# Kernel tuning notes

Hardware: AMD Instinct MI355X
Metric: run time of the kernel (lower is better)

## Reference

```python
import jax, jax.numpy as jnp
import numpy as np

N, M, B = 50000, 400000, 1000   # nodes, edges, graphs
F, E, G, P = 39, 11, 200, 128   # node feat, edge feat, graph feat, predictor dim
T = 2                            # readout timesteps


def _leaky(x):
    return jnp.where(x > 0, x, 0.01 * x)  # nn.LeakyReLU default slope


def _gru(x, h, wih, whh, bih, bhh):
    # torch.nn.GRUCell math; weights stored [in, 3H] so we use x @ W
    gx = x @ wih + bih
    gh = h @ whh + bhh
    xr, xz, xn = jnp.split(gx, 3, axis=-1)
    hr, hz, hn = jnp.split(gh, 3, axis=-1)
    r = jax.nn.sigmoid(xr + hr)
    z = jax.nn.sigmoid(xz + hz)
    n = jnp.tanh(xn + r * hn)
    return (1.0 - z) * n + z * h


def _seg_softmax(logits, seg, num):
    # softmax over entries sharing the same segment id (dgl edge_softmax / softmax_nodes)
    m = jax.ops.segment_max(logits, seg, num_segments=num)
    e = jnp.exp(logits - m[seg])
    s = jax.ops.segment_sum(e, seg, num_segments=num)
    return e / s[seg]


def setup_inputs() -> dict:
    key = jax.random.key(0)
    kit = iter(jax.random.split(key, 64))

    def rn(shape, scale=0.1):
        return jax.random.normal(next(kit), shape, dtype=jnp.float32) * scale

    inp = dict(
        node_feats=rn((N, F), 1.0),
        edge_feats=rn((M, E), 1.0),
        pn_w=rn((F, G)), pn_b=rn((G,)),
        pe1_w=rn((F + E, G)), pe1_b=rn((G,)),
        pe2_w=rn((2 * G, 1)), pe2_b=rn((1,)),
        et_w=rn((G, G)), et_b=rn((G,)),
        gru0_wih=rn((G, 3 * G)), gru0_whh=rn((G, 3 * G)),
        gru0_bih=rn((3 * G,)), gru0_bhh=rn((3 * G,)),
        lpe_w=rn((2 * G, 1)), lpe_b=rn((1,)),
        lpn_w=rn((G, G)), lpn_b=rn((G,)),
        gru1_wih=rn((G, 3 * G)), gru1_whh=rn((G, 3 * G)),
        gru1_bih=rn((3 * G,)), gru1_bhh=rn((3 * G,)),
        r_logit_w=rn((T, 2 * G, 1)), r_logit_b=rn((T, 1)),
        r_proj_w=rn((T, G, G)), r_proj_b=rn((T, G)),
        r_gru_wih=rn((T, G, 3 * G)), r_gru_whh=rn((T, G, 3 * G)),
        r_gru_bih=rn((T, 3 * G)), r_gru_bhh=rn((T, 3 * G)),
        t_w=rn((G, P)), t_b=rn((P,)),
        src=jax.random.randint(next(kit), (M,), 0, N, dtype=jnp.int32),
        dst=jax.random.randint(next(kit), (M,), 0, N, dtype=jnp.int32),
        graph_ids=(jnp.arange(N, dtype=jnp.int32) // (N // B)).astype(jnp.int32),
    )
    return inp


def reference(node_feats, edge_feats,
              pn_w, pn_b, pe1_w, pe1_b, pe2_w, pe2_b, et_w, et_b,
              gru0_wih, gru0_whh, gru0_bih, gru0_bhh,
              lpe_w, lpe_b, lpn_w, lpn_b,
              gru1_wih, gru1_whh, gru1_bih, gru1_bhh,
              r_logit_w, r_logit_b, r_proj_w, r_proj_b,
              r_gru_wih, r_gru_whh, r_gru_bih, r_gru_bhh,
              t_w, t_b, src, dst, graph_ids):
    n = node_feats.shape[0]
    # ---- GetContext (first AttentiveFPGNN layer) ----
    hv_new = _leaky(node_feats @ pn_w + pn_b)                                   # [N,G]
    he1 = _leaky(jnp.concatenate([node_feats[src], edge_feats], -1) @ pe1_w + pe1_b)  # [M,G]
    logits = _leaky(jnp.concatenate([hv_new[dst], he1], -1) @ pe2_w + pe2_b)    # [M,1]
    a = _seg_softmax(logits, dst, n)
    c = jax.ops.segment_sum(a * (he1 @ et_w + et_b), dst, num_segments=n)       # [N,G]
    h = jax.nn.relu(_gru(jax.nn.elu(c), hv_new, gru0_wih, gru0_whh, gru0_bih, gru0_bhh))
    # ---- GNNLayer (num_layers-1 = 1) ----
    logits = _leaky(jnp.concatenate([h[dst], h[src]], -1) @ lpe_w + lpe_b)      # [M,1]
    a = _seg_softmax(logits, dst, n)
    hv_proj = h @ lpn_w + lpn_b
    c = jax.ops.segment_sum(a * hv_proj[src], dst, num_segments=n)
    h = jax.nn.relu(_gru(jax.nn.elu(c), h, gru1_wih, gru1_whh, gru1_bih, gru1_bhh))
    # ---- AttentiveFPReadout ----
    g = jax.ops.segment_sum(h, graph_ids, num_segments=B)                        # [B,G]
    for t in range(T):
        z = _leaky(jnp.concatenate([jax.nn.relu(g)[graph_ids], h], -1) @ r_logit_w[t] + r_logit_b[t])
        a = _seg_softmax(z, graph_ids, B)                                        # [N,1]
        hv = h @ r_proj_w[t] + r_proj_b[t]
        g_repr = jax.ops.segment_sum(a * hv, graph_ids, num_segments=B)
        g = _gru(jax.nn.elu(g_repr), g, r_gru_wih[t], r_gru_whh[t], r_gru_bih[t], r_gru_bhh[t])
    # ---- final transform ----
    return g @ t_w + t_b                                                         # [B,P]
```

## Files before the change

### kernel.cpp

```cpp
#include <hip/hip_runtime.h>
#include <hip/hip_bf16.h>

#define NN 50000
#define MM 400000
#define BB 1000
#define FF 39
#define EE 11
#define GG 200
#define PP 128

typedef __attribute__((ext_vector_type(8))) short bf16x8;
typedef __attribute__((ext_vector_type(4))) float f32x4;
struct us4 { unsigned short x, y, z, w; };

__device__ __forceinline__ float bf2f(unsigned short u) {
  return __uint_as_float(((unsigned int)u) << 16);
}
__device__ __forceinline__ unsigned short f2bf(float x) {
  union { __hip_bfloat16 b; unsigned short u; } v;
  v.b = __float2bfloat16(x);
  return v.u;
}
__device__ __forceinline__ float leakyf(float x) { return x > 0.f ? x : 0.01f * x; }
__device__ __forceinline__ float eluf(float x)   { return x > 0.f ? x : (expf(x) - 1.f); }
__device__ __forceinline__ float sigmf(float x)  { return 1.f / (1.f + expf(-x)); }
__device__ __forceinline__ int sw(int row, int seg) {
  return row * 32 + ((seg ^ ((row >> 1) & 3)) << 3);
}
template <typename T> __device__ __forceinline__ float ldv(const T* p);
template <> __device__ __forceinline__ float ldv<float>(const float* p) { return *p; }
template <> __device__ __forceinline__ float ldv<unsigned short>(const unsigned short* p) { return bf2f(*p); }

template <typename T>
__device__ __forceinline__ void stage16(const T* ap, int kbase, int K, bool rowok, short* tmp) {
  if (rowok && kbase + 16 <= K) {
    if constexpr (sizeof(T) == 2) {
      *(bf16x8*)&tmp[0] = *(const bf16x8*)(ap);
      *(bf16x8*)&tmp[8] = *(const bf16x8*)(ap + 8);
    } else {
#pragma unroll
      for (int j = 0; j < 16; ++j) tmp[j] = (short)f2bf(ap[j]);
    }
  } else if (rowok) {
#pragma unroll
    for (int j = 0; j < 16; ++j) {
      if (kbase + j < K) {
        if constexpr (sizeof(T) == 2) tmp[j] = (short)ap[j];
        else tmp[j] = (short)f2bf(ap[j]);
      } else tmp[j] = 0;
    }
  } else {
#pragma unroll
    for (int j = 0; j < 16; ++j) tmp[j] = 0;
  }
}

__global__ __launch_bounds__(256) void detect_dtype(const unsigned int* __restrict__ w,
                                                    int* __restrict__ flag) {
  __shared__ int cnt[256];
  int c = 0;
  for (int i = threadIdx.x; i < 2048; i += 256) {
    unsigned int e = (w[i] >> 8) & 0x7F;
    c += (e >= 60 && e <= 64) ? 1 : 0;
  }
  cnt[threadIdx.x] = c;
  __syncthreads();
  for (int s = 128; s; s >>= 1) {
    if (threadIdx.x < s) cnt[threadIdx.x] += cnt[threadIdx.x + s];
    __syncthreads();
  }
  if (threadIdx.x == 0) *flag = (cnt[0] >= 1024) ? 1 : 0;
}

struct CvtJob { const void* s; float* d; int n; int pad; };
struct CvtJobs32 { CvtJob j[32]; };

__global__ __launch_bounds__(256) void cvt_any(CvtJobs32 jobs, const int* __restrict__ flag) {
  CvtJob job = jobs.j[blockIdx.y];
  int isbf = *flag;
  if (isbf) {
    const unsigned short* s = (const unsigned short*)job.s;
    for (int i = blockIdx.x * 256 + threadIdx.x; i < job.n; i += gridDim.x * 256)
      job.d[i] = bf2f(s[i]);
  } else {
    const float* s = (const float*)job.s;
    for (int i = blockIdx.x * 256 + threadIdx.x; i < job.n; i += gridDim.x * 256)
      job.d[i] = s[i];
  }
}

struct TJob { const float* s; unsigned short* d; int K; int N; };
struct TJobs12 { TJob j[12]; };

__global__ __launch_bounds__(256) void transpose_bf16(TJobs12 jobs) {
  TJob job = jobs.j[blockIdx.y];
  int total = job.K * job.N;
  for (int idx = blockIdx.x * 256 + threadIdx.x; idx < total; idx += gridDim.x * 256) {
    int n = idx / job.K, k = idx - n * job.K;
    job.d[idx] = f2bf(job.s[(size_t)k * job.N + n]);
  }
}

__global__ __launch_bounds__(256) void hist_kernel(const int* __restrict__ dst,
                                                   int* __restrict__ cnt, int M) {
  int e = blockIdx.x * 256 + threadIdx.x;
  if (e < M) atomicAdd(&cnt[dst[e]], 1);
}

#define SCHUNK 2048
__global__ __launch_bounds__(256) void scan1_kernel(const int* __restrict__ cnt,
                                                    int* __restrict__ incl,
                                                    int* __restrict__ bsum, int n) {
  __shared__ int lds[256];
  int b = blockIdx.x, tid = threadIdx.x;
  int base = b * SCHUNK + tid * 8;
  int v[8], s = 0;
#pragma unroll
  for (int j = 0; j < 8; ++j) { int i = base + j; v[j] = (i < n) ? cnt[i] : 0; s += v[j]; }
  lds[tid] = s;
  __syncthreads();
  for (int o = 1; o < 256; o <<= 1) {
    int t = (tid >= o) ? lds[tid - o] : 0;
    __syncthreads();
    lds[tid] += t;
    __syncthreads();
  }
  int run = lds[tid] - s;
#pragma unroll
  for (int j = 0; j < 8; ++j) {
    run += v[j];
    int i = base + j;
    if (i < n) incl[i] = run;
  }
  if (tid == 255) bsum[b] = lds[255];
}

__global__ void scan2_kernel(int* __restrict__ bsum, int nb) {
  if (threadIdx.x == 0 && blockIdx.x == 0) {
    int run = 0;
    for (int i = 0; i < nb; ++i) { int t = bsum[i]; bsum[i] = run; run += t; }
  }
}

__global__ __launch_bounds__(256) void scan3_kernel(const int* __restrict__ incl,
                                                    const int* __restrict__ cnt,
                                                    const int* __restrict__ bsum,
                                                    int* __restrict__ offA,
                                                    int* __restrict__ cur, int n) {
  int i = blockIdx.x * 256 + threadIdx.x;
  if (i >= n) return;
  int o = incl[i] - cnt[i] + bsum[i / SCHUNK];
  offA[i] = o;
  cur[i] = o;
}

__global__ __launch_bounds__(256) void fill_kernel(const int* __restrict__ dst,
                                                   int* __restrict__ cur,
                                                   int* __restrict__ elist, int M) {
  int e = blockIdx.x * 256 + threadIdx.x;
  if (e >= M) return;
  int pos = atomicAdd(&cur[dst[e]], 1);
  elist[pos] = e;
}

__global__ __launch_bounds__(64) void l1_agg(
    const float* __restrict__ Xe, const unsigned short* __restrict__ xa,
    const unsigned short* __restrict__ hvnew,
    const float* __restrict__ pe1w_e, const float* __restrict__ pe1b,
    const float* __restrict__ pe2w_n, const float* __restrict__ pe2w_e,
    const float* __restrict__ pe2b, const int* __restrict__ srcA,
    const int* __restrict__ offA, const int* __restrict__ cntA, const int* __restrict__ elist,
    unsigned short* __restrict__ S, float* __restrict__ ssumOut, int N)
{
  int v = blockIdx.x;
  int lane = threadIdx.x;
  if (v >= N) return;
  int begin = offA[v], cnt = cntA[v];
  bool act = lane < 50;
  int kb = act ? 4 * lane : 0;
  float b[4], p[4], pn[4];
  float pw[EE][4];
#pragma unroll
// ... 70 lines not shown
    float h2 = bf2f(g0.z) + b[2], h3 = bf2f(g0.w) + b[3];
#pragma unroll
    for (int jj = 0; jj < EE; ++jj) {
      float x = Xe[(size_t)e0 * EE + jj];
      h0 += x * pw[jj][0]; h1 += x * pw[jj][1];
      h2 += x * pw[jj][2]; h3 += x * pw[jj][3];
    }
    h0 = leakyf(h0); h1 = leakyf(h1); h2 = leakyf(h2); h3 = leakyf(h3);
    float bp = h0 * p[0] + h1 * p[1] + h2 * p[2] + h3 * p[3];
#pragma unroll
    for (int o = 32; o; o >>= 1) bp += __shfl_down(bp, o);
    float w = __expf(fminf(leakyf(alv + __shfl(bp, 0)), 60.f));
    ss += w;
    a0 += w * h0; a1 += w * h1; a2 += w * h2; a3 += w * h3;
  }
  float inv = (cnt > 0) ? 1.f / ss : 0.f;
  if (act) {
    us4 o4;
    o4.x = f2bf(a0 * inv); o4.y = f2bf(a1 * inv);
    o4.z = f2bf(a2 * inv); o4.w = f2bf(a3 * inv);
    *(us4*)(S + (size_t)v * GG + kb) = o4;
  }
  if (lane == 0) ssumOut[v] = (cnt > 0) ? ss : 0.f;
}

__global__ __launch_bounds__(64) void l2_agg(
    const unsigned short* __restrict__ hvp, const float* __restrict__ gd,
    const float* __restrict__ gs, const float* __restrict__ lpeb,
    const int* __restrict__ srcA,
    const int* __restrict__ offA, const int* __restrict__ cntA, const int* __restrict__ elist,
    unsigned short* __restrict__ S2, int N)
{
  int v = blockIdx.x;
  int lane = threadIdx.x;
  if (v >= N) return;
  int begin = offA[v], cnt = cntA[v];
  bool act = lane < 50;
  int kb = act ? 4 * lane : 0;
  float gdv = gd[v] + lpeb[0];
  float ss = 0.f;
  float a0 = 0.f, a1 = 0.f, a2 = 0.f, a3 = 0.f;
  int t = 0;
  for (; t + 4 <= cnt; t += 4) {
    int e[4], s[4];
#pragma unroll
    for (int u = 0; u < 4; ++u) {
      e[u] = __builtin_amdgcn_readfirstlane(elist[begin + t + u]);
      s[u] = __builtin_amdgcn_readfirstlane(srcA[e[u]]);
    }
    us4 g0 = *(const us4*)(hvp + (size_t)s[0] * GG + kb);
    us4 g1 = *(const us4*)(hvp + (size_t)s[1] * GG + kb);
    us4 g2 = *(const us4*)(hvp + (size_t)s[2] * GG + kb);
    us4 g3 = *(const us4*)(hvp + (size_t)s[3] * GG + kb);
    float w0 = __expf(fminf(leakyf(gdv + gs[s[0]]), 60.f));
    float w1 = __expf(fminf(leakyf(gdv + gs[s[1]]), 60.f));
    float w2 = __expf(fminf(leakyf(gdv + gs[s[2]]), 60.f));
    float w3 = __expf(fminf(leakyf(gdv + gs[s[3]]), 60.f));
    ss += w0 + w1 + w2 + w3;
    a0 += w0 * bf2f(g0.x) + w1 * bf2f(g1.x) + w2 * bf2f(g2.x) + w3 * bf2f(g3.x);
    a1 += w0 * bf2f(g0.y) + w1 * bf2f(g1.y) + w2 * bf2f(g2.y) + w3 * bf2f(g3.y);
    a2 += w0 * bf2f(g0.z) + w1 * bf2f(g1.z) + w2 * bf2f(g2.z) + w3 * bf2f(g3.z);
    a3 += w0 * bf2f(g0.w) + w1 * bf2f(g1.w) + w2 * bf2f(g2.w) + w3 * bf2f(g3.w);
  }
  for (; t < cnt; ++t) {
    int e = __builtin_amdgcn_readfirstlane(elist[begin + t]);
    int s = __builtin_amdgcn_readfirstlane(srcA[e]);
    us4 g = *(const us4*)(hvp + (size_t)s * GG + kb);
    float w = __expf(fminf(leakyf(gdv + gs[s]), 60.f));
    ss += w;
    a0 += w * bf2f(g.x); a1 += w * bf2f(g.y);
    a2 += w * bf2f(g.z); a3 += w * bf2f(g.w);
  }
  float inv = (cnt > 0) ? 1.f / ss : 0.f;
  if (act) {
    us4 o4;
    o4.x = f2bf((cnt > 0) ? eluf(a0 * inv) : 0.f);
    o4.y = f2bf((cnt > 0) ? eluf(a1 * inv) : 0.f);
    o4.z = f2bf((cnt > 0) ? eluf(a2 * inv) : 0.f);
    o4.w = f2bf((cnt > 0) ? eluf(a3 * inv) : 0.f);
    *(us4*)(S2 + (size_t)v * GG + kb) = o4;
  }
}

template <typename TA>
__global__ __launch_bounds__(256) void mfma_gemm(
    const TA* __restrict__ A, const unsigned short* __restrict__ Wt,
    const float* __restrict__ bias, const float* __restrict__ rowmask,
    unsigned short* __restrict__ Cb, int Mr, int Nc, int K, int act)
{
  __shared__ __attribute__((aligned(16))) short As[128 * 32];
  __shared__ __attribute__((aligned(16))) short Bs[64 * 32];
  int ncol = (Nc + 63) >> 6;
  int nrowt = (Mr + 127) >> 7;
  int per = 8 * ncol;
  int grp = blockIdx.x / per, rem = blockIdx.x % per;
  int rowt = grp * 8 + (rem & 7), colt = rem >> 3;
  if (rowt >= nrowt) return;
  int row0 = rowt * 128, col0 = colt * 64;
  int tid = threadIdx.x;
  int w = tid >> 6, lane = tid & 63, quad = lane >> 4, l15 = lane & 15;

  f32x4 zero4 = {0.f, 0.f, 0.f, 0.f};
  f32x4 acc[2][4];
#pragma unroll
  for (int r = 0; r < 2; ++r)
#pragma unroll
    for (int c = 0; c < 4; ++c) acc[r][c] = zero4;

  for (int k0 = 0; k0 < K; k0 += 32) {
    {
      int row = tid >> 1, half = tid & 1;
      int r = row0 + row;
      short tmp[16];
      stage16<TA>(A + (size_t)r * K + k0 + half * 16, k0 + half * 16, K, r < Mr, tmp);
      *(bf16x8*)&As[sw(row, 2 * half)]     = *(bf16x8*)&tmp[0];
      *(bf16x8*)&As[sw(row, 2 * half + 1)] = *(bf16x8*)&tmp[8];
    }
    {
      int col = tid & 63, seg = tid >> 6;
      int n = col0 + col, k = k0 + seg * 8;
      short t8[8];
      const unsigned short* wp = Wt + (size_t)n * K + k;
      if (n < Nc && k + 8 <= K) {
        *(bf16x8*)&t8[0] = *(const bf16x8*)wp;
      } else {
#pragma unroll
        for (int j = 0; j < 8; ++j)
          t8[j] = (n < Nc && k + j < K) ? (short)wp[j] : (short)0;
      }
      *(bf16x8*)&Bs[sw(col, seg)] = *(bf16x8*)&t8[0];
    }
    __syncthreads();
    bf16x8 a[2], b[4];
#pragma unroll
    for (int r = 0; r < 2; ++r)
      a[r] = *(const bf16x8*)&As[sw(w * 32 + r * 16 + l15, quad)];
#pragma unroll
    for (int c = 0; c < 4; ++c)
      b[c] = *(const bf16x8*)&Bs[sw(c * 16 + l15, quad)];
#pragma unroll
    for (int r = 0; r < 2; ++r)
#pragma unroll
      for (int c = 0; c < 4; ++c)
        acc[r][c] = __builtin_amdgcn_mfma_f32_16x16x32_bf16(a[r], b[c], acc[r][c], 0, 0, 0);
    __syncthreads();
  }
#pragma unroll
  for (int r = 0; r < 2; ++r) {
#pragma unroll
    for (int c = 0; c < 4; ++c) {
      int col = col0 + c * 16 + l15;
      if (col >= Nc) continue;
#pragma unroll
      for (int i = 0; i < 4; ++i) {
        int row = row0 + w * 32 + r * 16 + quad * 4 + i;
        if (row >= Mr) continue;
        bool valid = (rowmask == nullptr) || (rowmask[row] > 0.f);
        float v = valid ? (acc[r][c][i] + (bias ? bias[col] : 0.f)) : 0.f;
        if (act == 1) v = leakyf(v);
        else if (act == 2) v = eluf(v);
        Cb[(size_t)row * Nc + col] = f2bf(v);
      }
    }
  }
}

template <typename TI, typename TO>
__global__ __launch_bounds__(256) void mfma_gru(
    const TI* __restrict__ X, const TI* __restrict__ H,
    const unsigned short* __restrict__ WtIH, const unsigned short* __restrict__ WtHH,
    const float* __restrict__ bih, const float* __restrict__ bhh,
    TO* __restrict__ Out, int R, int relu_out)
{
  __shared__ __attribute__((aligned(16))) short Xs[128 * 32];
  __shared__ __attribute__((aligned(16))) short Hs[128 * 32];
  __shared__ __attribute__((aligned(16))) short Ws[192 * 32];
  int nrowt = (R + 127) >> 7;
  int grp = blockIdx.x / 56, rem = blockIdx.x % 56;
  int rowt = grp * 8 + (rem & 7), colt = rem >> 3;
  if (rowt >= nrowt) return;
  int row0 = rowt * 128, col0 = colt * 32;
  int tid = threadIdx.x;
  int w = tid >> 6, lane = tid & 63, quad = lane >> 4, l15 = lane & 15;

  f32x4 zero4 = {0.f, 0.f, 0.f, 0.f};
  f32x4 acc[6][2][2];
#pragma unroll
  for (int g = 0; g < 6; ++g)
#pragma unroll
    for (int r = 0; r < 2; ++r)
#pragma unroll
      for (int c = 0; c < 2; ++c) acc[g][r][c] = zero4;

  for (int k0 = 0; k0 < GG; k0 += 32) {
    {
      int row = tid >> 1, half = tid & 1;
      int r = row0 + row;
      short tx[16], th[16];
      stage16<TI>(X + (size_t)r * GG + k0 + half * 16, k0 + half * 16, GG, r < R, tx);
      stage16<TI>(H + (size_t)r * GG + k0 + half * 16, k0 + half * 16, GG, r < R, th);
      *(bf16x8*)&Xs[sw(row, 2 * half)]     = *(bf16x8*)&tx[0];
      *(bf16x8*)&Xs[sw(row, 2 * half + 1)] = *(bf16x8*)&tx[8];
      *(bf16x8*)&Hs[sw(row, 2 * half)]     = *(bf16x8*)&th[0];
      *(bf16x8*)&Hs[sw(row, 2 * half + 1)] = *(bf16x8*)&th[8];
    }
    for (int task = tid; task < 768; task += 256) {
      int rw = task >> 2, seg = task & 3;
      int g = rw >> 5, cc = rw & 31;
      int n = col0 + cc, k = k0 + seg * 8;
      const unsigned short* wp = (g < 3)
          ? WtIH + (size_t)(g * GG + n) * GG + k
          : WtHH + (size_t)((g - 3) * GG + n) * GG + k;
      short t8[8];
      if (n < GG && k + 8 <= GG) {
        *(bf16x8*)&t8[0] = *(const bf16x8*)wp;
      } else {
#pragma unroll
        for (int j = 0; j < 8; ++j)
          t8[j] = (n < GG && k + j < GG) ? (short)wp[j] : (short)0;
      }
      *(bf16x8*)&Ws[sw(rw, seg)] = *(bf16x8*)&t8[0];
    }
    __syncthreads();
    bf16x8 ax[2], ah[2];
#pragma unroll
    for (int r = 0; r < 2; ++r) {
      ax[r] = *(const bf16x8*)&Xs[sw(w * 32 + r * 16 + l15, quad)];
      ah[r] = *(const bf16x8*)&Hs[sw(w * 32 + r * 16 + l15, quad)];
    }
#pragma unroll
    for (int g = 0; g < 6; ++g) {
      bf16x8 b[2];
#pragma unroll
      for (int c = 0; c < 2; ++c)
        b[c] = *(const bf16x8*)&Ws[sw(g * 32 + c * 16 + l15, quad)];
#pragma unroll
      for (int r = 0; r < 2; ++r)
#pragma unroll
        for (int c = 0; c < 2; ++c)
          acc[g][r][c] = __builtin_amdgcn_mfma_f32_16x16x32_bf16(
              (g < 3) ? ax[r] : ah[r], b[c], acc[g][r][c], 0, 0, 0);
    }
    __syncthreads();
  }
#pragma unroll
  for (int r = 0; r < 2; ++r) {
#pragma unroll
    for (int c = 0; c < 2; ++c) {
      int col = col0 + c * 16 + l15;
      if (col >= GG) continue;
      float br = bih[col],       bhr = bhh[col];
      float bz = bih[200 + col], bhz = bhh[200 + col];
      float bn = bih[400 + col], bhn = bhh[400 + col];
#pragma unroll
      for (int i = 0; i < 4; ++i) {
        int row = row0 + w * 32 + r * 16 + quad * 4 + i;
        if (row >= R) continue;
        float rr = sigmf(acc[0][r][c][i] + br + acc[3][r][c][i] + bhr);
        float zz = sigmf(acc[1][r][c][i] + bz + acc[4][r][c][i] + bhz);
        float nn = tanhf(acc[2][r][c][i] + bn + rr * (acc[5][r][c][i] + bhn));
        float hval = ldv<TI>(H + (size_t)row * GG + col);
        float o = (1.f - zz) * nn + zz * hval;
        if (relu_out) o = fmaxf(o, 0.f);
        if constexpr (sizeof(TO) == 2) Out[(size_t)row * GG + col] = f2bf(o);
        else Out[(size_t)row * GG + col] = o;
      }
    }
  }
}

#define Bb 64
#define Bn 64
#define Bk 16
__global__ __launch_bounds__(256) void gemm_kernel(
    const float* __restrict__ A, const float* __restrict__ W,
    const float* __restrict__ bias, const float* __restrict__ rowmask,
    float* __restrict__ Cf, void* __restrict__ Oout, const int* __restrict__ oflag,
    int Mr, int Nc, int K, int act)
{
  __shared__ float As[Bk][Bb + 1];
  __shared__ float Ws[Bk][Bn];
  int row0 = blockIdx.x * Bb, col0 = blockIdx.y * Bn;
  int tid = threadIdx.x;
  int ty = tid >> 4, tx = tid & 15;
  float acc[4][4] = {};
  for (int k0 = 0; k0 < K; k0 += Bk) {
    for (int l = tid; l < Bb * Bk; l += 256) {
      int m = l >> 4, kk = l & 15;
      int r = row0 + m, k = k0 + kk;
      As[kk][m] = (r < Mr && k < K) ? A[(size_t)r * K + k] : 0.f;
    }
    for (int l = tid; l < Bk * Bn; l += 256) {
      int kk = l >> 6, nn = l & 63;
      int k = k0 + kk, c = col0 + nn;
      Ws[kk][nn] = (k < K && c < Nc) ? W[(size_t)k * Nc + c] : 0.f;
    }
    __syncthreads();
#pragma unroll
    for (int kk = 0; kk < Bk; ++kk) {
      float av[4], bv[4];
#pragma unroll
      for (int i = 0; i < 4; ++i) av[i] = As[kk][ty * 4 + i];
#pragma unroll
      for (int j = 0; j < 4; ++j) bv[j] = Ws[kk][tx * 4 + j];
#pragma unroll
      for (int i = 0; i < 4; ++i)
#pragma unroll
        for (int j = 0; j < 4; ++j) acc[i][j] += av[i] * bv[j];
    }
    __syncthreads();
  }
  int isbf = (oflag != nullptr) ? *oflag : 0;
#pragma unroll
  for (int i = 0; i < 4; ++i) {
    int r = row0 + ty * 4 + i;
    if (r >= Mr) continue;
    bool valid = (rowmask == nullptr) || (rowmask[r] > 0.f);
#pragma unroll
    for (int j = 0; j < 4; ++j) {
      int c = col0 + tx * 4 + j;
      if (c >= Nc) continue;
      float v = valid ? (acc[i][j] + (bias ? bias[c] : 0.f)) : 0.f;
      if (act == 1) v = leakyf(v);
      else if (act == 2) v = eluf(v);
      else if (act == 3) v = fmaxf(v, 0.f);
      size_t idx = (size_t)r * Nc + c;
// ... 10 lines not shown
__global__ __launch_bounds__(256) void node_dot2(
    const unsigned short* __restrict__ X, const float* __restrict__ w1,
    const float* __restrict__ w2,
    float* __restrict__ o1, float* __restrict__ o2, int N)
{
  int v = (blockIdx.x * 256 + threadIdx.x) >> 6;
  int lane = threadIdx.x & 63;
  if (v >= N) return;
  float d1 = 0.f, d2 = 0.f;
  for (int k = lane; k < GG; k += 64) {
    float x = bf2f(X[(size_t)v * GG + k]);
    d1 += x * w1[k];
    if (w2) d2 += x * w2[k];
  }
  for (int off = 32; off; off >>= 1) {
    d1 += __shfl_down(d1, off);
    if (w2) d2 += __shfl_down(d2, off);
  }
  if (lane == 0) { o1[v] = d1; if (w2) o2[v] = d2; }
}

__global__ __launch_bounds__(256) void graph_sum(
    const unsigned short* __restrict__ h, float* __restrict__ g)
{
  int b = blockIdx.x, k = threadIdx.x;
  if (k < GG) {
    float a = 0.f;
    for (int i = 0; i < 50; ++i) a += bf2f(h[((size_t)b * 50 + i) * GG + k]);
    g[(size_t)b * GG + k] = a;
  }
}

__global__ __launch_bounds__(256) void attn_kernel(
    const float* __restrict__ g, const unsigned short* __restrict__ h2,
    const float* __restrict__ w1, const float* __restrict__ dh,
    const float* __restrict__ rb, float* __restrict__ weighted)
{
  int b = blockIdx.x;
  __shared__ float red[256];
  __shared__ float zs[50];
  __shared__ float as_[50];
  __shared__ float dgs;
  int tid = threadIdx.x;
  float p = 0.f;
  if (tid < GG) p = fmaxf(g[(size_t)b * GG + tid], 0.f) * w1[tid];
  red[tid] = p;
  __syncthreads();
  for (int s = 128; s; s >>= 1) { if (tid < s) red[tid] += red[tid + s]; __syncthreads(); }
  if (tid == 0) dgs = red[0];
  __syncthreads();
  if (tid < 50) zs[tid] = leakyf(dgs + dh[b * 50 + tid] + rb[0]);
  __syncthreads();
  if (tid == 0) {
    float m = -1e30f;
    for (int i = 0; i < 50; ++i) m = fmaxf(m, zs[i]);
    float s = 0.f;
    for (int i = 0; i < 50; ++i) { float e = expf(zs[i] - m); as_[i] = e; s += e; }
    float inv = 1.f / s;
    for (int i = 0; i < 50; ++i) as_[i] *= inv;
  }
  __syncthreads();
  if (tid < GG) {
    float a = 0.f;
    for (int i = 0; i < 50; ++i) a += as_[i] * bf2f(h2[((size_t)b * 50 + i) * GG + tid]);
    weighted[(size_t)b * GG + tid] = a;
  }
}

static inline int gemm_grid(int Mr, int Nc) {
  int nrow = (Mr + 127) / 128, ncol = (Nc + 63) / 64;
  return ((nrow + 7) / 8) * 8 * ncol;
}
static inline int gru_grid(int R) {
  int nrow = (R + 127) / 128;
  return ((nrow + 7) / 8) * 56;
}

extern "C" void kernel_launch(void* const* d_in, const int* in_sizes, int n_in,
                              void* d_out, int out_size, void* d_ws, size_t ws_size,
                              hipStream_t stream)
{
  (void)n_in; (void)out_size; (void)ws_size;
  const int N = NN, M = MM, B = BB, F = FF, G = GG, P = PP;
  float* ws = (float*)d_ws;
  size_t off = 0;
  auto alloc = [&](size_t n) { size_t o = off; off += (n + 63) & ~(size_t)63; return o; };

  size_t o_flag = alloc(16);
  size_t o_pn_w = alloc(F * G), o_pn_b = alloc(G);
  size_t o_pe1_w = alloc((F + EE) * G), o_pe1_b = alloc(G);
  size_t o_pe2_w = alloc(2 * G), o_pe2_b = alloc(1);
  size_t o_et_w = alloc(G * G), o_et_b = alloc(G);
  size_t o_g0_wih = alloc(G * 3 * G), o_g0_whh = alloc(G * 3 * G);
  size_t o_g0_bih = alloc(3 * G), o_g0_bhh = alloc(3 * G);
  size_t o_lpe_w = alloc(2 * G), o_lpe_b = alloc(1);
  size_t o_lpn_w = alloc(G * G), o_lpn_b = alloc(G);
  size_t o_g1_wih = alloc(G * 3 * G), o_g1_whh = alloc(G * 3 * G);
  size_t o_g1_bih = alloc(3 * G), o_g1_bhh = alloc(3 * G);
  size_t o_rl_w = alloc(2 * 2 * G), o_rl_b = alloc(2);
  size_t o_rp_w = alloc(2 * G * G), o_rp_b = alloc(2 * G);
  size_t o_rg_wih = alloc(2 * G * 3 * G), o_rg_whh = alloc(2 * G * 3 * G);
  size_t o_rg_bih = alloc(2 * 3 * G), o_rg_bhh = alloc(2 * 3 * G);
  size_t o_t_w = alloc(G * P), o_t_b = alloc(P);
  size_t o_Xn = alloc((size_t)N * F);
  size_t o_Xe = alloc((size_t)M * EE);
  size_t o_B1 = alloc((size_t)N * G);
  size_t o_B2 = alloc((size_t)N * G);
  size_t o_B3 = alloc((size_t)N * G);
  size_t o_ssum = alloc(N);
  size_t o_gd = alloc(N), o_gs = alloc(N), o_dh = alloc(N);
  size_t o_gv0 = alloc((size_t)B * G), o_gwt = alloc((size_t)B * G), o_grep = alloc((size_t)B * G);
  size_t o_gv1 = alloc((size_t)B * G), o_gv2 = alloc((size_t)B * G);
  size_t o_etT  = alloc(G * G / 2), o_lpnT = alloc(G * G / 2);
  size_t o_g0ihT = alloc(G * 3 * G / 2), o_g0hhT = alloc(G * 3 * G / 2);
  size_t o_g1ihT = alloc(G * 3 * G / 2), o_g1hhT = alloc(G * 3 * G / 2);
  size_t o_rg0ihT = alloc(G * 3 * G / 2), o_rg0hhT = alloc(G * 3 * G / 2);
  size_t o_rg1ihT = alloc(G * 3 * G / 2), o_rg1hhT = alloc(G * 3 * G / 2);
  size_t o_pnT = alloc(G * F / 2 + 64), o_pe1T = alloc(G * F / 2 + 64);
  size_t o_cnt = alloc(N), o_off = alloc(N), o_cur = alloc(N);
  size_t o_elist = alloc(M), o_bsum = alloc(64), o_incl = alloc(N);

  int* flag = (int*)(ws + o_flag);
  int* cntA = (int*)(ws + o_cnt);
  int* offA = (int*)(ws + o_off);
  int* curA = (int*)(ws + o_cur);
  int* elist = (int*)(ws + o_elist);
  int* bsum = (int*)(ws + o_bsum);
  int* incl = (int*)(ws + o_incl);
  unsigned short* B1b = (unsigned short*)(ws + o_B1);
  unsigned short* B2b = (unsigned short*)(ws + o_B2);
  unsigned short* B3b = (unsigned short*)(ws + o_B3);

  CvtJobs32 jobs;
  int ji = 0;
  auto push = [&](int idx, size_t dsto) {
    jobs.j[ji].s = d_in[idx];
    jobs.j[ji].d = ws + dsto;
    jobs.j[ji].n = in_sizes[idx];
    jobs.j[ji].pad = 0;
    ++ji;
  };
  push(0, o_Xn);
  push(1, o_Xe);
  push(2, o_pn_w);  push(3, o_pn_b);
  push(4, o_pe1_w); push(5, o_pe1_b);
  push(6, o_pe2_w); push(7, o_pe2_b);
  push(8, o_et_w);  push(9, o_et_b);
  push(10, o_g0_wih); push(11, o_g0_whh); push(12, o_g0_bih); push(13, o_g0_bhh);
  push(14, o_lpe_w);  push(15, o_lpe_b);
  push(16, o_lpn_w);  push(17, o_lpn_b);
  push(18, o_g1_wih); push(19, o_g1_whh); push(20, o_g1_bih); push(21, o_g1_bhh);
  push(22, o_rl_w);   push(23, o_rl_b);
  push(24, o_rp_w);   push(25, o_rp_b);
  push(26, o_rg_wih); push(27, o_rg_whh); push(28, o_rg_bih); push(29, o_rg_bhh);
  push(30, o_t_w);    push(31, o_t_b);

  const int* src = (const int*)d_in[32];
  const int* dst = (const int*)d_in[33];

  dim3 blk(256);
  detect_dtype<<<dim3(1), blk, 0, stream>>>((const unsigned int*)d_in[0], flag);
  cvt_any<<<dim3(512, 32), blk, 0, stream>>>(jobs, flag);

  hipMemsetAsync(cntA, 0, (size_t)N * 4, stream);
  hist_kernel<<<dim3((M + 255) / 256), blk, 0, stream>>>(dst, cntA, M);
  int nscb = (N + SCHUNK - 1) / SCHUNK;
  scan1_kernel<<<dim3(nscb), blk, 0, stream>>>(cntA, incl, bsum, N);
  scan2_kernel<<<dim3(1), dim3(64), 0, stream>>>(bsum, nscb);
  scan3_kernel<<<dim3((N + 255) / 256), blk, 0, stream>>>(incl, cntA, bsum, offA, curA, N);
  fill_kernel<<<dim3((M + 255) / 256), blk, 0, stream>>>(dst, curA, elist, M);

  TJobs12 tj;
  auto tpush = [&](int slot, size_t srcO, size_t dstO, int K, int Nc) {
    tj.j[slot].s = ws + srcO;
    tj.j[slot].d = (unsigned short*)(ws + dstO);
    tj.j[slot].K = K; tj.j[slot].N = Nc;
  };
  tpush(0, o_et_w,  o_etT,  G, G);
  tpush(1, o_lpn_w, o_lpnT, G, G);
  tpush(2, o_g0_wih, o_g0ihT, G, 3 * G);
  tpush(3, o_g0_whh, o_g0hhT, G, 3 * G);
  tpush(4, o_g1_wih, o_g1ihT, G, 3 * G);
  tpush(5, o_g1_whh, o_g1hhT, G, 3 * G);
  tpush(6, o_rg_wih, o_rg0ihT, G, 3 * G);
  tpush(7, o_rg_whh, o_rg0hhT, G, 3 * G);
  tpush(8, o_rg_wih + (size_t)G * 3 * G, o_rg1ihT, G, 3 * G);
  tpush(9, o_rg_whh + (size_t)G * 3 * G, o_rg1hhT, G, 3 * G);
  tpush(10, o_pn_w,  o_pnT,  F, G);
  tpush(11, o_pe1_w, o_pe1T, F, G);
  transpose_bf16<<<dim3(128, 12), blk, 0, stream>>>(tj);

  mfma_gemm<float><<<dim3(gemm_grid(N, G)), blk, 0, stream>>>(
      ws + o_Xn, (const unsigned short*)(ws + o_pnT), ws + o_pn_b, nullptr,
      B1b, N, G, F, 1);
  mfma_gemm<float><<<dim3(gemm_grid(N, G)), blk, 0, stream>>>(
      ws + o_Xn, (const unsigned short*)(ws + o_pe1T), nullptr, nullptr,
      B2b, N, G, F, 0);
  l1_agg<<<dim3(N), dim3(64), 0, stream>>>(ws + o_Xe, B2b, B1b,
                                           ws + o_pe1_w + (size_t)F * G, ws + o_pe1_b,
                                           ws + o_pe2_w, ws + o_pe2_w + G, ws + o_pe2_b,
                                           src, offA, cntA, elist,
                                           B3b, ws + o_ssum, N);
  mfma_gemm<unsigned short><<<dim3(gemm_grid(N, G)), blk, 0, stream>>>(
      B3b, (const unsigned short*)(ws + o_etT), ws + o_et_b, ws + o_ssum,
      B2b, N, G, G, 2);
  mfma_gru<unsigned short, unsigned short><<<dim3(gru_grid(N)), blk, 0, stream>>>(
      B2b, B1b,
      (const unsigned short*)(ws + o_g0ihT), (const unsigned short*)(ws + o_g0hhT),
      ws + o_g0_bih, ws + o_g0_bhh, B3b, N, 1);

  dim3 gWave((N + 3) / 4);
  node_dot2<<<gWave, blk, 0, stream>>>(B3b, ws + o_lpe_w, ws + o_lpe_w + G,
                                       ws + o_gd, ws + o_gs, N);
  mfma_gemm<unsigned short><<<dim3(gemm_grid(N, G)), blk, 0, stream>>>(
      B3b, (const unsigned short*)(ws + o_lpnT), ws + o_lpn_b, nullptr,
      B1b, N, G, G, 0);
  l2_agg<<<dim3(N), dim3(64), 0, stream>>>(B1b, ws + o_gd, ws + o_gs, ws + o_lpe_b,
                                           src, offA, cntA, elist, B2b, N);
  mfma_gru<unsigned short, unsigned short><<<dim3(gru_grid(N)), blk, 0, stream>>>(
      B2b, B3b,
      (const unsigned short*)(ws + o_g1ihT), (const unsigned short*)(ws + o_g1hhT),
      ws + o_g1_bih, ws + o_g1_bhh, B1b, N, 1);

  graph_sum<<<dim3(B), blk, 0, stream>>>(B1b, ws + o_gv0);
  dim3 gBG((B + Bb - 1) / Bb, (G + Bn - 1) / Bn);
  size_t gcur = o_gv0, gnext = o_gv1;
  for (int t = 0; t < 2; ++t) {
    node_dot2<<<gWave, blk, 0, stream>>>(B1b, ws + o_rl_w + t * 2 * G + G,
                                         nullptr, ws + o_dh, nullptr, N);
    attn_kernel<<<dim3(B), blk, 0, stream>>>(ws + gcur, B1b, ws + o_rl_w + t * 2 * G,
                                             ws + o_dh, ws + o_rl_b + t, ws + o_gwt);
    gemm_kernel<<<gBG, blk, 0, stream>>>(ws + o_gwt, ws + o_rp_w + (size_t)t * G * G,
                                         ws + o_rp_b + t * G, nullptr,
                                         ws + o_grep, nullptr, nullptr, B, G, G, 2);
    mfma_gru<float, float><<<dim3(gru_grid(B)), blk, 0, stream>>>(
        ws + o_grep, ws + gcur,
        (const unsigned short*)(ws + (t == 0 ? o_rg0ihT : o_rg1ihT)),
        (const unsigned short*)(ws + (t == 0 ? o_rg0hhT : o_rg1hhT)),
        ws + o_rg_bih + t * 3 * G, ws + o_rg_bhh + t * 3 * G,
        ws + gnext, B, 0);
    gcur = gnext;
    gnext = o_gv2;
  }
  dim3 gOut((B + Bb - 1) / Bb, (P + Bn - 1) / Bn);
  gemm_kernel<<<gOut, blk, 0, stream>>>(ws + gcur, ws + o_t_w, ws + o_t_b, nullptr,
                                        nullptr, d_out, flag, B, P, G, 0);
}
```

Baseline: 948.8 us.

## Load MFMA fragments directly from global memory with zero-padded transposed weights

The node GEMM and GRU kernels drop their LDS staging buffers and barriers. Each lane now loads its A and B MFMA fragments straight from global memory. Transposed weights are zero-padded to a multiple of 32 along K, and node features are pre-converted to padded bf16, so the inner loop needs no bounds checks. In exchange, fragment loads are less coalesced and rely on L2 for weight reuse. A-side reads past K pick up neighbouring row data, which only cancels because the padded weights are zero, and the last row can read past its buffer.

```diff
diff --git a/kernel.cpp b/kernel.cpp
--- a/kernel.cpp
+++ b/kernel.cpp
@@ -24,34 +24,23 @@
 __device__ __forceinline__ float leakyf(float x) { return x > 0.f ? x : 0.01f * x; }
 __device__ __forceinline__ float eluf(float x)   { return x > 0.f ? x : (expf(x) - 1.f); }
 __device__ __forceinline__ float sigmf(float x)  { return 1.f / (1.f + expf(-x)); }
-__device__ __forceinline__ int sw(int row, int seg) {
-  return row * 32 + ((seg ^ ((row >> 1) & 3)) << 3);
-}
 template <typename T> __device__ __forceinline__ float ldv(const T* p);
 template <> __device__ __forceinline__ float ldv<float>(const float* p) { return *p; }
 template <> __device__ __forceinline__ float ldv<unsigned short>(const unsigned short* p) { return bf2f(*p); }
 
 template <typename T>
-__device__ __forceinline__ void stage16(const T* ap, int kbase, int K, bool rowok, short* tmp) {
-  if (rowok && kbase + 16 <= K) {
-    if constexpr (sizeof(T) == 2) {
-      *(bf16x8*)&tmp[0] = *(const bf16x8*)(ap);
-      *(bf16x8*)&tmp[8] = *(const bf16x8*)(ap + 8);
-    } else {
-#pragma unroll
-      for (int j = 0; j < 16; ++j) tmp[j] = (short)f2bf(ap[j]);
-    }
-  } else if (rowok) {
-#pragma unroll
-    for (int j = 0; j < 16; ++j) {
-      if (kbase + j < K) {
-        if constexpr (sizeof(T) == 2) tmp[j] = (short)ap[j];
-        else tmp[j] = (short)f2bf(ap[j]);
-      } else tmp[j] = 0;
-    }
+__device__ __forceinline__ bf16x8 afrag(const T* base, size_t off) {
+  if constexpr (sizeof(T) == 2) {
+    return *(const bf16x8*)(base + off);
   } else {
-#pragma unroll
-    for (int j = 0; j < 16; ++j) tmp[j] = 0;
+    float4 f0 = *(const float4*)(base + off);
+    float4 f1 = *(const float4*)(base + off + 4);
+    short t[8];
+    t[0] = (short)f2bf(f0.x); t[1] = (short)f2bf(f0.y);
+    t[2] = (short)f2bf(f0.z); t[3] = (short)f2bf(f0.w);
+    t[4] = (short)f2bf(f1.x); t[5] = (short)f2bf(f1.y);
+    t[6] = (short)f2bf(f1.z); t[7] = (short)f2bf(f1.w);
+    return *(bf16x8*)t;
   }
 }
 
@@ -89,15 +78,31 @@
   }
 }
 
-struct TJob { const float* s; unsigned short* d; int K; int N; };
+__global__ __launch_bounds__(256) void cvt_xn(const void* __restrict__ src,
+                                              unsigned short* __restrict__ dstb,
+                                              const int* __restrict__ flag, int N) {
+  int isbf = *flag;
+  int total = N * 40;
+  for (int i = blockIdx.x * 256 + threadIdx.x; i < total; i += gridDim.x * 256) {
+    int n = i / 40, k = i - n * 40;
+    unsigned short v = 0;
+    if (k < FF) {
+      if (isbf) v = ((const unsigned short*)src)[n * FF + k];
+      else      v = f2bf(((const float*)src)[n * FF + k]);
+    }
+    dstb[i] = v;
+  }
+}
+
+struct TJob { const float* s; unsigned short* d; int K; int N; int KP; int pad; };
 struct TJobs12 { TJob j[12]; };
 
 __global__ __launch_bounds__(256) void transpose_bf16(TJobs12 jobs) {
   TJob job = jobs.j[blockIdx.y];
-  int total = job.K * job.N;
+  int total = job.N * job.KP;
   for (int idx = blockIdx.x * 256 + threadIdx.x; idx < total; idx += gridDim.x * 256) {
-    int n = idx / job.K, k = idx - n * job.K;
-    job.d[idx] = f2bf(job.s[(size_t)k * job.N + n]);
+    int n = idx / job.KP, k = idx - n * job.KP;
+    job.d[idx] = (k < job.K) ? f2bf(job.s[(size_t)k * job.N + n]) : (unsigned short)0;
   }
 }
 
@@ -334,14 +339,12 @@
   }
 }
 
-template <typename TA>
-__global__ __launch_bounds__(256) void mfma_gemm(
-    const TA* __restrict__ A, const unsigned short* __restrict__ Wt,
+__global__ __launch_bounds__(256) void mfma_gemm_d(
+    const unsigned short* __restrict__ A, int strideA,
+    const unsigned short* __restrict__ Wt, int KP,
     const float* __restrict__ bias, const float* __restrict__ rowmask,
-    unsigned short* __restrict__ Cb, int Mr, int Nc, int K, int act)
-{
-  __shared__ __attribute__((aligned(16))) short As[128 * 32];
-  __shared__ __attribute__((aligned(16))) short Bs[64 * 32];
+    unsigned short* __restrict__ Cb, int Mr, int Nc, int act)
+{
   int ncol = (Nc + 63) >> 6;
   int nrowt = (Mr + 127) >> 7;
   int per = 8 * ncol;
@@ -352,6 +355,12 @@
   int tid = threadIdx.x;
   int w = tid >> 6, lane = tid & 63, quad = lane >> 4, l15 = lane & 15;
 
+  int rA0 = min(row0 + w * 32 + l15, Mr - 1);
+  int rA1 = min(row0 + w * 32 + 16 + l15, Mr - 1);
+  int nB[4];
+#pragma unroll
+  for (int c = 0; c < 4; ++c) nB[c] = min(col0 + c * 16 + l15, Nc - 1);
+
   f32x4 zero4 = {0.f, 0.f, 0.f, 0.f};
   f32x4 acc[2][4];
 #pragma unroll
@@ -359,43 +368,18 @@
 #pragma unroll
     for (int c = 0; c < 4; ++c) acc[r][c] = zero4;
 
-  for (int k0 = 0; k0 < K; k0 += 32) {
-    {
-      int row = tid >> 1, half = tid & 1;
-      int r = row0 + row;
-      short tmp[16];
-      stage16<TA>(A + (size_t)r * K + k0 + half * 16, k0 + half * 16, K, r < Mr, tmp);
-      *(bf16x8*)&As[sw(row, 2 * half)]     = *(bf16x8*)&tmp[0];
-      *(bf16x8*)&As[sw(row, 2 * half + 1)] = *(bf16x8*)&tmp[8];
-    }
-    {
-      int col = tid & 63, seg = tid >> 6;
-      int n = col0 + col, k = k0 + seg * 8;
-      short t8[8];
-      const unsigned short* wp = Wt + (size_t)n * K + k;
-      if (n < Nc && k + 8 <= K) {
-        *(bf16x8*)&t8[0] = *(const bf16x8*)wp;
-      } else {
-#pragma unroll
-        for (int j = 0; j < 8; ++j)
-          t8[j] = (n < Nc && k + j < K) ? (short)wp[j] : (short)0;
-      }
-      *(bf16x8*)&Bs[sw(col, seg)] = *(bf16x8*)&t8[0];
-    }
-    __syncthreads();
-    bf16x8 a[2], b[4];
-#pragma unroll
-    for (int r = 0; r < 2; ++r)
-      a[r] = *(const bf16x8*)&As[sw(w * 32 + r * 16 + l15, quad)];
-#pragma unroll
-    for (int c = 0; c < 4; ++c)
-      b[c] = *(const bf16x8*)&Bs[sw(c * 16 + l15, quad)];
-#pragma unroll
-    for (int r = 0; r < 2; ++r)
-#pragma unroll
-      for (int c = 0; c < 4; ++c)
-        acc[r][c] = __builtin_amdgcn_mfma_f32_16x16x32_bf16(a[r], b[c], acc[r][c], 0, 0, 0);
-    __syncthreads();
+  for (int k0 = 0; k0 < KP; k0 += 32) {
+    int kq = k0 + quad * 8;
+    bf16x8 a0 = afrag(A, (size_t)rA0 * strideA + kq);
+    bf16x8 a1 = afrag(A, (size_t)rA1 * strideA + kq);
+    bf16x8 b[4];
+#pragma unroll
+    for (int c = 0; c < 4; ++c) b[c] = afrag(Wt, (size_t)nB[c] * KP + kq);
+#pragma unroll
+    for (int c = 0; c < 4; ++c) {
+      acc[0][c] = __builtin_amdgcn_mfma_f32_16x16x32_bf16(a0, b[c], acc[0][c], 0, 0, 0);
+      acc[1][c] = __builtin_amdgcn_mfma_f32_16x16x32_bf16(a1, b[c], acc[1][c], 0, 0, 0);
+    }
   }
 #pragma unroll
   for (int r = 0; r < 2; ++r) {
@@ -418,15 +402,12 @@
 }
 
 template <typename TI, typename TO>
-__global__ __launch_bounds__(256) void mfma_gru(
+__global__ __launch_bounds__(256) void mfma_gru_d(
     const TI* __restrict__ X, const TI* __restrict__ H,
     const unsigned short* __restrict__ WtIH, const unsigned short* __restrict__ WtHH,
-    const float* __restrict__ bih, const float* __restrict__ bhh,
+    int KP, const float* __restrict__ bih, const float* __restrict__ bhh,
     TO* __restrict__ Out, int R, int relu_out)
 {
-  __shared__ __attribute__((aligned(16))) short Xs[128 * 32];
-  __shared__ __attribute__((aligned(16))) short Hs[128 * 32];
-  __shared__ __attribute__((aligned(16))) short Ws[192 * 32];
   int nrowt = (R + 127) >> 7;
   int grp = blockIdx.x / 56, rem = blockIdx.x % 56;
   int rowt = grp * 8 + (rem & 7), colt = rem >> 3;
@@ -435,6 +416,11 @@
   int tid = threadIdx.x;
   int w = tid >> 6, lane = tid & 63, quad = lane >> 4, l15 = lane & 15;
 
+  int rA0 = min(row0 + w * 32 + l15, R - 1);
+  int rA1 = min(row0 + w * 32 + 16 + l15, R - 1);
+  int nB0 = min(col0 + l15, GG - 1);
+  int nB1 = min(col0 + 16 + l15, GG - 1);
+
   f32x4 zero4 = {0.f, 0.f, 0.f, 0.f};
   f32x4 acc[6][2][2];
 #pragma unroll
@@ -444,56 +430,27 @@
 #pragma unroll
       for (int c = 0; c < 2; ++c) acc[g][r][c] = zero4;
 
-  for (int k0 = 0; k0 < GG; k0 += 32) {
-    {
-      int row = tid >> 1, half = tid & 1;
-      int r = row0 + row;
-      short tx[16], th[16];
-      stage16<TI>(X + (size_t)r * GG + k0 + half * 16, k0 + half * 16, GG, r < R, tx);
-      stage16<TI>(H + (size_t)r * GG + k0 + half * 16, k0 + half * 16, GG, r < R, th);
-      *(bf16x8*)&Xs[sw(row, 2 * half)]     = *(bf16x8*)&tx[0];
-      *(bf16x8*)&Xs[sw(row, 2 * half + 1)] = *(bf16x8*)&tx[8];
-      *(bf16x8*)&Hs[sw(row, 2 * half)]     = *(bf16x8*)&th[0];
-      *(bf16x8*)&Hs[sw(row, 2 * half + 1)] = *(bf16x8*)&th[8];
-    }
-    for (int task = tid; task < 768; task += 256) {
-      int rw = task >> 2, seg = task & 3;
-      int g = rw >> 5, cc = rw & 31;
-      int n = col0 + cc, k = k0 + seg * 8;
-      const unsigned short* wp = (g < 3)
-          ? WtIH + (size_t)(g * GG + n) * GG + k
-          : WtHH + (size_t)((g - 3) * GG + n) * GG + k;
-      short t8[8];
-      if (n < GG && k + 8 <= GG) {
-        *(bf16x8*)&t8[0] = *(const bf16x8*)wp;
-      } else {
-#pragma unroll
-        for (int j = 0; j < 8; ++j)
-          t8[j] = (n < GG && k + j < GG) ? (short)wp[j] : (short)0;
-      }
-      *(bf16x8*)&Ws[sw(rw, seg)] = *(bf16x8*)&t8[0];
-    }
-    __syncthreads();
-    bf16x8 ax[2], ah[2];
-#pragma unroll
-    for (int r = 0; r < 2; ++r) {
-      ax[r] = *(const bf16x8*)&Xs[sw(w * 32 + r * 16 + l15, quad)];
-      ah[r] = *(const bf16x8*)&Hs[sw(w * 32 + r * 16 + l15, quad)];
-    }
-#pragma unroll
-    for (int g = 0; g < 6; ++g) {
-      bf16x8 b[2];
-#pragma unroll
-      for (int c = 0; c < 2; ++c)
-        b[c] = *(const bf16x8*)&Ws[sw(g * 32 + c * 16 + l15, quad)];
-#pragma unroll
-      for (int r = 0; r < 2; ++r)
-#pragma unroll
-        for (int c = 0; c < 2; ++c)
-          acc[g][r][c] = __builtin_amdgcn_mfma_f32_16x16x32_bf16(
-              (g < 3) ? ax[r] : ah[r], b[c], acc[g][r][c], 0, 0, 0);
-    }
-    __syncthreads();
+  for (int k0 = 0; k0 < KP; k0 += 32) {
+    int kq = k0 + quad * 8;
+    bf16x8 ax0 = afrag(X, (size_t)rA0 * GG + kq);
+    bf16x8 ax1 = afrag(X, (size_t)rA1 * GG + kq);
+    bf16x8 ah0 = afrag(H, (size_t)rA0 * GG + kq);
+    bf16x8 ah1 = afrag(H, (size_t)rA1 * GG + kq);
+#pragma unroll
+    for (int g = 0; g < 3; ++g) {
+      bf16x8 bi0 = afrag(WtIH, (size_t)(g * GG + nB0) * KP + kq);
+      bf16x8 bi1 = afrag(WtIH, (size_t)(g * GG + nB1) * KP + kq);
+      bf16x8 bh0 = afrag(WtHH, (size_t)(g * GG + nB0) * KP + kq);
+      bf16x8 bh1 = afrag(WtHH, (size_t)(g * GG + nB1) * KP + kq);
+      acc[g][0][0] = __builtin_amdgcn_mfma_f32_16x16x32_bf16(ax0, bi0, acc[g][0][0], 0, 0, 0);
+      acc[g][0][1] = __builtin_amdgcn_mfma_f32_16x16x32_bf16(ax0, bi1, acc[g][0][1], 0, 0, 0);
+      acc[g][1][0] = __builtin_amdgcn_mfma_f32_16x16x32_bf16(ax1, bi0, acc[g][1][0], 0, 0, 0);
+      acc[g][1][1] = __builtin_amdgcn_mfma_f32_16x16x32_bf16(ax1, bi1, acc[g][1][1], 0, 0, 0);
+      acc[g + 3][0][0] = __builtin_amdgcn_mfma_f32_16x16x32_bf16(ah0, bh0, acc[g + 3][0][0], 0, 0, 0);
+      acc[g + 3][0][1] = __builtin_amdgcn_mfma_f32_16x16x32_bf16(ah0, bh1, acc[g + 3][0][1], 0, 0, 0);
+      acc[g + 3][1][0] = __builtin_amdgcn_mfma_f32_16x16x32_bf16(ah1, bh0, acc[g + 3][1][0], 0, 0, 0);
+      acc[g + 3][1][1] = __builtin_amdgcn_mfma_f32_16x16x32_bf16(ah1, bh1, acc[g + 3][1][1], 0, 0, 0);
+    }
   }
 #pragma unroll
   for (int r = 0; r < 2; ++r) {
@@ -670,6 +627,7 @@
 {
   (void)n_in; (void)out_size; (void)ws_size;
   const int N = NN, M = MM, B = BB, F = FF, G = GG, P = PP;
+  const int KP200 = 224, KP39 = 64;
   float* ws = (float*)d_ws;
   size_t off = 0;
   auto alloc = [&](size_t n) { size_t o = off; off += (n + 63) & ~(size_t)63; return o; };
@@ -690,7 +648,7 @@
   size_t o_rg_wih = alloc(2 * G * 3 * G), o_rg_whh = alloc(2 * G * 3 * G);
   size_t o_rg_bih = alloc(2 * 3 * G), o_rg_bhh = alloc(2 * 3 * G);
   size_t o_t_w = alloc(G * P), o_t_b = alloc(P);
-  size_t o_Xn = alloc((size_t)N * F);
+  size_t o_Xnb = alloc((size_t)N * 40 / 2 + 64);
   size_t o_Xe = alloc((size_t)M * EE);
   size_t o_B1 = alloc((size_t)N * G);
   size_t o_B2 = alloc((size_t)N * G);
@@ -699,12 +657,12 @@
   size_t o_gd = alloc(N), o_gs = alloc(N), o_dh = alloc(N);
   size_t o_gv0 = alloc((size_t)B * G), o_gwt = alloc((size_t)B * G), o_grep = alloc((size_t)B * G);
   size_t o_gv1 = alloc((size_t)B * G), o_gv2 = alloc((size_t)B * G);
-  size_t o_etT  = alloc(G * G / 2), o_lpnT = alloc(G * G / 2);
-  size_t o_g0ihT = alloc(G * 3 * G / 2), o_g0hhT = alloc(G * 3 * G / 2);
-  size_t o_g1ihT = alloc(G * 3 * G / 2), o_g1hhT = alloc(G * 3 * G / 2);
-  size_t o_rg0ihT = alloc(G * 3 * G / 2), o_rg0hhT = alloc(G * 3 * G / 2);
-  size_t o_rg1ihT = alloc(G * 3 * G / 2), o_rg1hhT = alloc(G * 3 * G / 2);
-  size_t o_pnT = alloc(G * F / 2 + 64), o_pe1T = alloc(G * F / 2 + 64);
+  size_t o_etT  = alloc(G * KP200 / 2 + 64), o_lpnT = alloc(G * KP200 / 2 + 64);
+  size_t o_g0ihT = alloc(3 * G * KP200 / 2 + 64), o_g0hhT = alloc(3 * G * KP200 / 2 + 64);
+  size_t o_g1ihT = alloc(3 * G * KP200 / 2 + 64), o_g1hhT = alloc(3 * G * KP200 / 2 + 64);
+  size_t o_rg0ihT = alloc(3 * G * KP200 / 2 + 64), o_rg0hhT = alloc(3 * G * KP200 / 2 + 64);
+  size_t o_rg1ihT = alloc(3 * G * KP200 / 2 + 64), o_rg1hhT = alloc(3 * G * KP200 / 2 + 64);
+  size_t o_pnT = alloc(G * KP39 / 2 + 64), o_pe1T = alloc(G * KP39 / 2 + 64);
   size_t o_cnt = alloc(N), o_off = alloc(N), o_cur = alloc(N);
   size_t o_elist = alloc(M), o_bsum = alloc(64), o_incl = alloc(N);
 
@@ -715,6 +673,7 @@
   int* elist = (int*)(ws + o_elist);
   int* bsum = (int*)(ws + o_bsum);
   int* incl = (int*)(ws + o_incl);
+  unsigned short* Xnb = (unsigned short*)(ws + o_Xnb);
   unsigned short* B1b = (unsigned short*)(ws + o_B1);
   unsigned short* B2b = (unsigned short*)(ws + o_B2);
   unsigned short* B3b = (unsigned short*)(ws + o_B3);
@@ -728,7 +687,6 @@
     jobs.j[ji].pad = 0;
     ++ji;
   };
-  push(0, o_Xn);
   push(1, o_Xe);
   push(2, o_pn_w);  push(3, o_pn_b);
   push(4, o_pe1_w); push(5, o_pe1_b);
@@ -748,7 +706,8 @@
 
   dim3 blk(256);
   detect_dtype<<<dim3(1), blk, 0, stream>>>((const unsigned int*)d_in[0], flag);
-  cvt_any<<<dim3(512, 32), blk, 0, stream>>>(jobs, flag);
+  cvt_any<<<dim3(512, 31), blk, 0, stream>>>(jobs, flag);
+  cvt_xn<<<dim3((N * 40 + 255) / 256), blk, 0, stream>>>(d_in[0], Xnb, flag, N);
 
   hipMemsetAsync(cntA, 0, (size_t)N * 4, stream);
   hist_kernel<<<dim3((M + 255) / 256), blk, 0, stream>>>(dst, cntA, M);
@@ -759,55 +718,56 @@
   fill_kernel<<<dim3((M + 255) / 256), blk, 0, stream>>>(dst, curA, elist, M);
 
   TJobs12 tj;
-  auto tpush = [&](int slot, size_t srcO, size_t dstO, int K, int Nc) {
+  auto tpush = [&](int slot, size_t srcO, size_t dstO, int K, int Nc, int KPv) {
     tj.j[slot].s = ws + srcO;
     tj.j[slot].d = (unsigned short*)(ws + dstO);
-    tj.j[slot].K = K; tj.j[slot].N = Nc;
+    tj.j[slot].K = K; tj.j[slot].N = Nc; tj.j[slot].KP = KPv; tj.j[slot].pad = 0;
   };
-  tpush(0, o_et_w,  o_etT,  G, G);
-  tpush(1, o_lpn_w, o_lpnT, G, G);
-  tpush(2, o_g0_wih, o_g0ihT, G, 3 * G);
-  tpush(3, o_g0_whh, o_g0hhT, G, 3 * G);
-  tpush(4, o_g1_wih, o_g1ihT, G, 3 * G);
-  tpush(5, o_g1_whh, o_g1hhT, G, 3 * G);
-  tpush(6, o_rg_wih, o_rg0ihT, G, 3 * G);
-  tpush(7, o_rg_whh, o_rg0hhT, G, 3 * G);
-  tpush(8, o_rg_wih + (size_t)G * 3 * G, o_rg1ihT, G, 3 * G);
-  tpush(9, o_rg_whh + (size_t)G * 3 * G, o_rg1hhT, G, 3 * G);
-  tpush(10, o_pn_w,  o_pnT,  F, G);
-  tpush(11, o_pe1_w, o_pe1T, F, G);
+  tpush(0, o_et_w,  o_etT,  G, G, KP200);
+  tpush(1, o_lpn_w, o_lpnT, G, G, KP200);
+  tpush(2, o_g0_wih, o_g0ihT, G, 3 * G, KP200);
+  tpush(3, o_g0_whh, o_g0hhT, G, 3 * G, KP200);
+  tpush(4, o_g1_wih, o_g1ihT, G, 3 * G, KP200);
+  tpush(5, o_g1_whh, o_g1hhT, G, 3 * G, KP200);
+  tpush(6, o_rg_wih, o_rg0ihT, G, 3 * G, KP200);
+  tpush(7, o_rg_whh, o_rg0hhT, G, 3 * G, KP200);
+  tpush(8, o_rg_wih + (size_t)G * 3 * G, o_rg1ihT, G, 3 * G, KP200);
+  tpush(9, o_rg_whh + (size_t)G * 3 * G, o_rg1hhT, G, 3 * G, KP200);
+  tpush(10, o_pn_w,  o_pnT,  F, G, KP39);
+  tpush(11, o_pe1_w, o_pe1T, F, G, KP39);
   transpose_bf16<<<dim3(128, 12), blk, 0, stream>>>(tj);
 
-  mfma_gemm<float><<<dim3(gemm_grid(N, G)), blk, 0, stream>>>(
-      ws + o_Xn, (const unsigned short*)(ws + o_pnT), ws + o_pn_b, nullptr,
-      B1b, N, G, F, 1);
-  mfma_gemm<float><<<dim3(gemm_grid(N, G)), blk, 0, stream>>>(
-      ws + o_Xn, (const unsigned short*)(ws + o_pe1T), nullptr, nullptr,
-      B2b, N, G, F, 0);
+  int gg = gemm_grid(N, G);
+  mfma_gemm_d<<<dim3(gg), blk, 0, stream>>>(
+      Xnb, 40, (const unsigned short*)(ws + o_pnT), KP39,
+      ws + o_pn_b, nullptr, B1b, N, G, 1);
+  mfma_gemm_d<<<dim3(gg), blk, 0, stream>>>(
+      Xnb, 40, (const unsigned short*)(ws + o_pe1T), KP39,
+      nullptr, nullptr, B2b, N, G, 0);
   l1_agg<<<dim3(N), dim3(64), 0, stream>>>(ws + o_Xe, B2b, B1b,
                                            ws + o_pe1_w + (size_t)F * G, ws + o_pe1_b,
                                            ws + o_pe2_w, ws + o_pe2_w + G, ws + o_pe2_b,
                                            src, offA, cntA, elist,
                                            B3b, ws + o_ssum, N);
-  mfma_gemm<unsigned short><<<dim3(gemm_grid(N, G)), blk, 0, stream>>>(
-      B3b, (const unsigned short*)(ws + o_etT), ws + o_et_b, ws + o_ssum,
-      B2b, N, G, G, 2);
-  mfma_gru<unsigned short, unsigned short><<<dim3(gru_grid(N)), blk, 0, stream>>>(
+  mfma_gemm_d<<<dim3(gg), blk, 0, stream>>>(
+      B3b, G, (const unsigned short*)(ws + o_etT), KP200,
+      ws + o_et_b, ws + o_ssum, B2b, N, G, 2);
+  mfma_gru_d<unsigned short, unsigned short><<<dim3(gru_grid(N)), blk, 0, stream>>>(
       B2b, B1b,
-      (const unsigned short*)(ws + o_g0ihT), (const unsigned short*)(ws + o_g0hhT),
+      (const unsigned short*)(ws + o_g0ihT), (const unsigned short*)(ws + o_g0hhT), KP200,
       ws + o_g0_bih, ws + o_g0_bhh, B3b, N, 1);
 
   dim3 gWave((N + 3) / 4);
   node_dot2<<<gWave, blk, 0, stream>>>(B3b, ws + o_lpe_w, ws + o_lpe_w + G,
                                        ws + o_gd, ws + o_gs, N);
-  mfma_gemm<unsigned short><<<dim3(gemm_grid(N, G)), blk, 0, stream>>>(
-      B3b, (const unsigned short*)(ws + o_lpnT), ws + o_lpn_b, nullptr,
-      B1b, N, G, G, 0);
+  mfma_gemm_d<<<dim3(gg), blk, 0, stream>>>(
+      B3b, G, (const unsigned short*)(ws + o_lpnT), KP200,
+      ws + o_lpn_b, nullptr, B1b, N, G, 0);
   l2_agg<<<dim3(N), dim3(64), 0, stream>>>(B1b, ws + o_gd, ws + o_gs, ws + o_lpe_b,
                                            src, offA, cntA, elist, B2b, N);
-  mfma_gru<unsigned short, unsigned short><<<dim3(gru_grid(N)), blk, 0, stream>>>(
+  mfma_gru_d<unsigned short, unsigned short><<<dim3(gru_grid(N)), blk, 0, stream>>>(
       B2b, B3b,
-      (const unsigned short*)(ws + o_g1ihT), (const unsigned short*)(ws + o_g1hhT),
+      (const unsigned short*)(ws + o_g1ihT), (const unsigned short*)(ws + o_g1hhT), KP200,
       ws + o_g1_bih, ws + o_g1_bhh, B1b, N, 1);
 
   graph_sum<<<dim3(B), blk, 0, stream>>>(B1b, ws + o_gv0);
@@ -821,10 +781,10 @@
     gemm_kernel<<<gBG, blk, 0, stream>>>(ws + o_gwt, ws + o_rp_w + (size_t)t * G * G,
                                          ws + o_rp_b + t * G, nullptr,
                                          ws + o_grep, nullptr, nullptr, B, G, G, 2);
-    mfma_gru<float, float><<<dim3(gru_grid(B)), blk, 0, stream>>>(
+    mfma_gru_d<float, float><<<dim3(gru_grid(B)), blk, 0, stream>>>(
         ws + o_grep, ws + gcur,
         (const unsigned short*)(ws + (t == 0 ? o_rg0ihT : o_rg1ihT)),
-        (const unsigned short*)(ws + (t == 0 ? o_rg0hhT : o_rg1hhT)),
+        (const unsigned short*)(ws + (t == 0 ? o_rg0hhT : o_rg1hhT)), KP200,
         ws + o_rg_bih + t * 3 * G, ws + o_rg_bhh + t * 3 * G,
         ws + gnext, B, 0);
     gcur = gnext;
```

New measurement: 910.8 us. 4.0% less time.
